# Optimization experiments

Measured on AMD Instinct MI355X. Metric: run time of the kernel, lower is better.

## Reference

```python
import jax, jax.numpy as jnp
import numpy as np

jax.config.update("jax_enable_x64", True)

P = 2038074743          # prime used by the ROBE-Z hash
BLOCK_K = 32            # tile sizes of the hashed reconstruction (kernel tile)
BLOCK_N = 32
INPUT_DIM = 8192
OUTPUT_DIM = 8192
HASH_SIZE = 1 << 22     # compressed parameter count
TOKENS = 512


def setup_inputs() -> dict:
    key = jax.random.key(0)
    k1, k2 = jax.random.split(key, 2)
    x = jax.random.normal(k1, (TOKENS, INPUT_DIM), dtype=jnp.float32)
    hashed_weight = jax.random.normal(k2, (HASH_SIZE,), dtype=jnp.float32) * 0.02
    bias = jnp.zeros((OUTPUT_DIM,), dtype=jnp.float32)
    # mirrors RzLinear._generate_random_numbers(seed): 4 random ints made even, prepended with P
    rng = np.random.RandomState(1024)
    r = rng.randint(0, P, size=(4,)).astype(np.int64)
    r = r + (r % 2)
    random_numbers = jnp.asarray(np.concatenate([np.array([P], dtype=np.int64), r]), dtype=jnp.int64)
    return {"x": x, "hashed_weight": hashed_weight, "bias": bias, "random_numbers": random_numbers}


def _weight_indices(random_numbers):
    """Hashed flat indices into hashed_weight for the dense [K, N] weight."""
    K, N = INPUT_DIM, OUTPUT_DIM
    kt, nt = K // BLOCK_K, N // BLOCK_N
    R1, R2, R3 = random_numbers[1], random_numbers[2], random_numbers[3]
    k_ids = jnp.arange(kt, dtype=jnp.int64)
    n_ids = jnp.arange(nt, dtype=jnp.int64)
    # per-tile start offset into the compressed array
    start = ((k_ids[:, None] * R3 + n_ids[None, :] * R2 + R1) % P) % (HASH_SIZE - BLOCK_K * BLOCK_N + 1)
    start = start.astype(jnp.int32)  # [kt, nt]
    off = (jnp.arange(BLOCK_K, dtype=jnp.int32)[:, None] * BLOCK_N
           + jnp.arange(BLOCK_N, dtype=jnp.int32)[None, :])  # [BK, BN], row-major within tile
    idx = start[:, None, :, None] + off[None, :, None, :]    # [kt, BK, nt, BN]
    return idx.reshape(K, N)


def reference(x, hashed_weight, bias, random_numbers):
    idx = _weight_indices(random_numbers)          # [K, N] int32
    W = hashed_weight[idx]                          # hashed-gather reconstruction, [K, N]
    out = jnp.matmul(x, W) + bias[None, :]          # [tokens, N]
    return out
```

## Files before the change

kernel.cpp:

```cpp
#include <hip/hip_runtime.h>
#include <hip/hip_fp16.h>

#define NDIM 8192
#define KDIM 8192
#define NT 256
#define MOD2 4193281
#define PRIME 2038074743LL

#define BM 256
#define BN 128
#define BK 32
#define KITER 64
#define ASTRIDE 40
#define BSLAB 1032

typedef _Float16 half8 __attribute__((ext_vector_type(8)));
typedef float floatx4 __attribute__((ext_vector_type(4)));

#define BARRIER() asm volatile("s_waitcnt lgkmcnt(0)\n\ts_barrier" ::: "memory")

__global__ __launch_bounds__(256) void prep_kernel(const float* __restrict__ x,
                                                   const float* __restrict__ hw,
                                                   const float* __restrict__ bias,
                                                   const int* __restrict__ rn,
                                                   __half* __restrict__ xh,
                                                   __half* __restrict__ hh,
                                                   int* __restrict__ starts,
                                                   float* __restrict__ out) {
    int b = blockIdx.x;
    int tid = threadIdx.x;
    if (b < 8192) {
        int i = b * 256 + tid;
        const float4* s; __half2* d; int j;
        if (i < (1 << 20)) { s = (const float4*)x;  d = (__half2*)xh; j = i; }
        else               { s = (const float4*)hw; d = (__half2*)hh; j = i - (1 << 20); }
        float4 v = s[j];
        d[j * 2]     = __floats2half2_rn(v.x, v.y);
        d[j * 2 + 1] = __floats2half2_rn(v.z, v.w);
    } else if (b < 8192 + 4096) {
        int i = (b - 8192) * 256 + tid;
        float4 bv = *(const float4*)(bias + ((i & 2047) << 2));
        ((float4*)out)[i] = bv;
    } else {
        int t = (b - 12288) * 256 + tid;
        bool is64 = (rn[1] == 0 && rn[3] == 0);
        long long R1 = is64 ? rn[2] : rn[1];
        long long R2 = is64 ? rn[4] : rn[2];
        long long R3 = is64 ? rn[6] : rn[3];
        long long k_id = t >> 8, n_id = t & 255;
        long long v = (k_id * R3 + n_id * R2 + R1) % PRIME;
        starts[t] = (int)(v % MOD2);
    }
}

__global__ __launch_bounds__(512, 4) void gemm_kernel(
    const __half* __restrict__ xh, const __half* __restrict__ hh,
    const int* __restrict__ starts, float* __restrict__ out) {
    __shared__ __align__(16) __half As[2][BM * ASTRIDE];
    __shared__ __align__(16) __half Bs[2][4 * BSLAB];
    __shared__ int Ss[KITER * 4];

    const int tid = threadIdx.x;
    const int lane = tid & 63;
    const int wave = tid >> 6;
    const int wm = wave >> 1;
    const int wn = wave & 1;
    const int quad = lane >> 4;
    const int l16 = lane & 15;

    const int i = blockIdx.x;
    const int ks = i & 3;
    const int m_blk = (i >> 2) & 1;
    const int n_blk = i >> 3;
    const int gm0 = m_blk * BM;
    const int gn0 = n_blk * BN;
    const int kt0 = ks * KITER;
    const int n_id0 = n_blk * 4;

    if (tid < KITER * 4) {
        int kp = tid >> 2, tile = tid & 3;
        Ss[tid] = starts[(kt0 + kp) * NT + n_id0 + tile];
    }

    const int a_row = tid >> 2;
    const int a_ch = tid & 3;
    const __half* aptr = xh + (size_t)(gm0 + a_row) * KDIM + kt0 * 32 + a_ch * 8;
    const unsigned a_woff = a_row * ASTRIDE + a_ch * 8;

    const int b_tile = tid >> 7;
    const int t7 = tid & 127;
    const int b_np = t7 & 15;
    const int b_kg = t7 >> 4;
    const int b_oct = b_kg >> 1;
    const unsigned b_woff = b_oct * BSLAB + (b_tile * 32 + 2 * b_np) * 8 + (b_kg & 1) * 4;

    uint4 paA0, paA1, paB0, paB1;
    unsigned pbA0, pbA1, pbA2, pbA3, pbB0, pbB1, pbB2, pbB3;

#define LOADT(P0, P1, Q0, Q1, Q2, Q3, kp_) do {                                \
        P0 = *(const uint4*)(aptr + (kp_) * 32);                               \
        P1 = *(const uint4*)(aptr + (size_t)128 * KDIM + (kp_) * 32);          \
        int st = Ss[(kp_) * 4 + b_tile];                                       \
        const __half* src = hh + st + b_kg * 128 + b_np * 2;                   \
        Q0 = *(const unsigned*)(src);                                          \
        Q1 = *(const unsigned*)(src + 32);                                     \
        Q2 = *(const unsigned*)(src + 64);                                     \
        Q3 = *(const unsigned*)(src + 96);                                     \
    } while (0)

#define STORET(P0, P1, Q0, Q1, Q2, Q3, buf_) do {                              \
        *(uint4*)&As[buf_][a_woff] = P0;                                       \
        *(uint4*)&As[buf_][(a_woff) + 128 * ASTRIDE] = P1;                     \
        unsigned lo0 = (Q0 & 0xffffu) | (Q1 << 16);                            \
        unsigned lo1 = (Q2 & 0xffffu) | (Q3 << 16);                            \
        unsigned hi0 = (Q0 >> 16) | (Q1 & 0xffff0000u);                        \
        unsigned hi1 = (Q2 >> 16) | (Q3 & 0xffff0000u);                        \
        uint2 e = {lo0, lo1}, o = {hi0, hi1};                                  \
        *(uint2*)&Bs[buf_][b_woff] = e;                                        \
        *(uint2*)&Bs[buf_][b_woff + 8] = o;                                    \
    } while (0)

    floatx4 acc[4][4];
#pragma unroll
    for (int r = 0; r < 4; r++)
#pragma unroll
        for (int c = 0; c < 4; c++)
            acc[r][c] = (floatx4){0.f, 0.f, 0.f, 0.f};

#define FRAGS_MFMA(buf_) do {                                                  \
        half8 af[4], bf[4];                                                    \
        _Pragma("unroll")                                                      \
        for (int r = 0; r < 4; r++)                                            \
            af[r] = *(const half8*)&As[buf_][(wm * 64 + r * 16 + l16) * ASTRIDE + quad * 8]; \
        _Pragma("unroll")                                                      \
        for (int c = 0; c < 4; c++)                                            \
            bf[c] = *(const half8*)&Bs[buf_][quad * BSLAB + (wn * 64 + c * 16 + l16) * 8];   \
        _Pragma("unroll")                                                      \
        for (int r = 0; r < 4; r++)                                            \
            _Pragma("unroll")                                                  \
            for (int c = 0; c < 4; c++)                                        \
                acc[r][c] = __builtin_amdgcn_mfma_f32_16x16x32_f16(af[r], bf[c], acc[r][c], 0, 0, 0); \
    } while (0)

    BARRIER();
    LOADT(paA0, paA1, pbA0, pbA1, pbA2, pbA3, 0);
    LOADT(paB0, paB1, pbB0, pbB1, pbB2, pbB3, 1);
    STORET(paA0, paA1, pbA0, pbA1, pbA2, pbA3, 0);
    BARRIER();

    for (int kp = 0; kp < KITER; kp += 2) {
        if (kp + 2 < KITER) LOADT(paA0, paA1, pbA0, pbA1, pbA2, pbA3, kp + 2);
        FRAGS_MFMA(0);
        STORET(paB0, paB1, pbB0, pbB1, pbB2, pbB3, 1);
        BARRIER();

        if (kp + 3 < KITER) LOADT(paB0, paB1, pbB0, pbB1, pbB2, pbB3, kp + 3);
        FRAGS_MFMA(1);
        if (kp + 2 < KITER)
            STORET(paA0, paA1, pbA0, pbA1, pbA2, pbA3, 0);
        BARRIER();
    }

#pragma unroll
    for (int c = 0; c < 4; c++) {
        int col = gn0 + wn * 64 + c * 16 + l16;
#pragma unroll
        for (int r = 0; r < 4; r++) {
            int row0 = gm0 + wm * 64 + r * 16 + quad * 4;
#pragma unroll
            for (int e = 0; e < 4; e++)
                atomicAdd(&out[(size_t)(row0 + e) * NDIM + col], acc[r][c][e]);
        }
    }
#undef LOADT
#undef STORET
#undef FRAGS_MFMA
}

extern "C" void kernel_launch(void* const* d_in, const int* in_sizes, int n_in,
                              void* d_out, int out_size, void* d_ws, size_t ws_size,
                              hipStream_t stream) {
    const float* x = (const float*)d_in[0];
    const float* hw = (const float*)d_in[1];
    const float* bias = (const float*)d_in[2];
    const int* rn = (const int*)d_in[3];
    float* out = (float*)d_out;

    char* ws = (char*)d_ws;
    __half* xh = (__half*)ws;
    __half* hh = (__half*)(ws + (8u << 20));
    int* starts = (int*)(ws + (16u << 20));

    hipLaunchKernelGGL(prep_kernel, dim3(12544), dim3(256), 0, stream,
                       x, hw, bias, rn, xh, hh, starts, out);
    hipLaunchKernelGGL(gemm_kernel, dim3(512), dim3(512), 0, stream, xh, hh, starts, out);
}
```

Before: 202.1 us.

## Halve GEMM block tile to 128x128 with 256 threads and restructure load pipeline

Shrinks the GEMM block tile from 256x128 to 128x128 and uses 256 threads per block, so the grid grows to 1024 blocks. The per-thread A and B load mapping is reorganized: A loads are split out and issued one step ahead, and each thread gathers eight hashed B values per tile stage and writes 16-byte LDS stores. The prep kernel now writes half-precision output as a single 8-byte store. This is meant to improve occupancy and CU load balance and to cut LDS store instruction count. In exchange, each B tile is fetched by twice as many blocks, and the separate A prefetch adds register pressure.

New measurement: 202.7 us. About the same (+0.3%).

```diff
diff --git a/kernel.cpp b/kernel.cpp
--- a/kernel.cpp
+++ b/kernel.cpp
@@ -7,7 +7,7 @@
 #define MOD2 4193281
 #define PRIME 2038074743LL
 
-#define BM 256
+#define BM 128
 #define BN 128
 #define BK 32
 #define KITER 64
@@ -31,12 +31,14 @@
     int tid = threadIdx.x;
     if (b < 8192) {
         int i = b * 256 + tid;
-        const float4* s; __half2* d; int j;
-        if (i < (1 << 20)) { s = (const float4*)x;  d = (__half2*)xh; j = i; }
-        else               { s = (const float4*)hw; d = (__half2*)hh; j = i - (1 << 20); }
+        const float4* s; uint2* d; int j;
+        if (i < (1 << 20)) { s = (const float4*)x;  d = (uint2*)xh; j = i; }
+        else               { s = (const float4*)hw; d = (uint2*)hh; j = i - (1 << 20); }
         float4 v = s[j];
-        d[j * 2]     = __floats2half2_rn(v.x, v.y);
-        d[j * 2 + 1] = __floats2half2_rn(v.z, v.w);
+        __half2 h01 = __floats2half2_rn(v.x, v.y);
+        __half2 h23 = __floats2half2_rn(v.z, v.w);
+        uint2 w = {*(unsigned*)&h01, *(unsigned*)&h23};
+        d[j] = w;
     } else if (b < 8192 + 4096) {
         int i = (b - 8192) * 256 + tid;
         float4 bv = *(const float4*)(bias + ((i & 2047) << 2));
@@ -53,7 +55,7 @@
     }
 }
 
-__global__ __launch_bounds__(512, 4) void gemm_kernel(
+__global__ __launch_bounds__(256, 4) void gemm_kernel(
     const __half* __restrict__ xh, const __half* __restrict__ hh,
     const int* __restrict__ starts, float* __restrict__ out) {
     __shared__ __align__(16) __half As[2][BM * ASTRIDE];
@@ -70,54 +72,60 @@
 
     const int i = blockIdx.x;
     const int ks = i & 3;
-    const int m_blk = (i >> 2) & 1;
-    const int n_blk = i >> 3;
+    const int m_blk = (i >> 2) & 3;
+    const int n_blk = i >> 4;
     const int gm0 = m_blk * BM;
     const int gn0 = n_blk * BN;
     const int kt0 = ks * KITER;
     const int n_id0 = n_blk * 4;
 
-    if (tid < KITER * 4) {
-        int kp = tid >> 2, tile = tid & 3;
-        Ss[tid] = starts[(kt0 + kp) * NT + n_id0 + tile];
-    }
-
-    const int a_row = tid >> 2;
-    const int a_ch = tid & 3;
-    const __half* aptr = xh + (size_t)(gm0 + a_row) * KDIM + kt0 * 32 + a_ch * 8;
-    const unsigned a_woff = a_row * ASTRIDE + a_ch * 8;
-
-    const int b_tile = tid >> 7;
-    const int t7 = tid & 127;
-    const int b_np = t7 & 15;
-    const int b_kg = t7 >> 4;
-    const int b_oct = b_kg >> 1;
-    const unsigned b_woff = b_oct * BSLAB + (b_tile * 32 + 2 * b_np) * 8 + (b_kg & 1) * 4;
-
-    uint4 paA0, paA1, paB0, paB1;
-    unsigned pbA0, pbA1, pbA2, pbA3, pbB0, pbB1, pbB2, pbB3;
-
-#define LOADT(P0, P1, Q0, Q1, Q2, Q3, kp_) do {                                \
-        P0 = *(const uint4*)(aptr + (kp_) * 32);                               \
-        P1 = *(const uint4*)(aptr + (size_t)128 * KDIM + (kp_) * 32);          \
+    Ss[tid] = starts[(kt0 + (tid >> 2)) * NT + n_id0 + (tid & 3)];
+
+    const int a_row = tid >> 1;
+    const int a_ch = tid & 1;
+    const __half* aptr = xh + (size_t)(gm0 + a_row) * KDIM + kt0 * 32 + a_ch * 16;
+    const unsigned a_woff = a_row * ASTRIDE + a_ch * 16;
+
+    const int b_tile = tid >> 6;
+    const int b_oct = (tid >> 4) & 3;
+    const int b_np = tid & 15;
+    const unsigned b_woff = b_oct * BSLAB + (b_tile * 32 + 2 * b_np) * 8;
+
+    uint4 pa0, pa1;
+    unsigned qE0, qE1, qE2, qE3, qE4, qE5, qE6, qE7;
+    unsigned qO0, qO1, qO2, qO3, qO4, qO5, qO6, qO7;
+
+#define LOADA(kp_) do {                                                        \
+        pa0 = *(const uint4*)(aptr + (kp_) * 32);                              \
+        pa1 = *(const uint4*)(aptr + (kp_) * 32 + 8);                          \
+    } while (0)
+
+#define LOADB(Q0, Q1, Q2, Q3, Q4, Q5, Q6, Q7, kp_) do {                        \
         int st = Ss[(kp_) * 4 + b_tile];                                       \
-        const __half* src = hh + st + b_kg * 128 + b_np * 2;                   \
+        const __half* src = hh + st + b_oct * 256 + b_np * 2;                  \
         Q0 = *(const unsigned*)(src);                                          \
         Q1 = *(const unsigned*)(src + 32);                                     \
         Q2 = *(const unsigned*)(src + 64);                                     \
         Q3 = *(const unsigned*)(src + 96);                                     \
-    } while (0)
-
-#define STORET(P0, P1, Q0, Q1, Q2, Q3, buf_) do {                              \
-        *(uint4*)&As[buf_][a_woff] = P0;                                       \
-        *(uint4*)&As[buf_][(a_woff) + 128 * ASTRIDE] = P1;                     \
-        unsigned lo0 = (Q0 & 0xffffu) | (Q1 << 16);                            \
-        unsigned lo1 = (Q2 & 0xffffu) | (Q3 << 16);                            \
-        unsigned hi0 = (Q0 >> 16) | (Q1 & 0xffff0000u);                        \
-        unsigned hi1 = (Q2 >> 16) | (Q3 & 0xffff0000u);                        \
-        uint2 e = {lo0, lo1}, o = {hi0, hi1};                                  \
-        *(uint2*)&Bs[buf_][b_woff] = e;                                        \
-        *(uint2*)&Bs[buf_][b_woff + 8] = o;                                    \
+        Q4 = *(const unsigned*)(src + 128);                                    \
+        Q5 = *(const unsigned*)(src + 160);                                    \
+        Q6 = *(const unsigned*)(src + 192);                                    \
+        Q7 = *(const unsigned*)(src + 224);                                    \
+    } while (0)
+
+#define STORET(Q0, Q1, Q2, Q3, Q4, Q5, Q6, Q7, buf_) do {                      \
+        *(uint4*)&As[buf_][a_woff] = pa0;                                      \
+        *(uint4*)&As[buf_][a_woff + 8] = pa1;                                  \
+        unsigned e0 = (Q0 & 0xffffu) | (Q1 << 16);                             \
+        unsigned e1 = (Q2 & 0xffffu) | (Q3 << 16);                             \
+        unsigned e2 = (Q4 & 0xffffu) | (Q5 << 16);                             \
+        unsigned e3 = (Q6 & 0xffffu) | (Q7 << 16);                             \
+        unsigned o0 = (Q0 >> 16) | (Q1 & 0xffff0000u);                         \
+        unsigned o1 = (Q2 >> 16) | (Q3 & 0xffff0000u);                         \
+        unsigned o2 = (Q4 >> 16) | (Q5 & 0xffff0000u);                         \
+        unsigned o3 = (Q6 >> 16) | (Q7 & 0xffff0000u);                         \
+        *(uint4*)&Bs[buf_][b_woff] = (uint4){e0, e1, e2, e3};                  \
+        *(uint4*)&Bs[buf_][b_woff + 8] = (uint4){o0, o1, o2, o3};              \
     } while (0)
 
     floatx4 acc[4][4];
@@ -143,21 +151,28 @@
     } while (0)
 
     BARRIER();
-    LOADT(paA0, paA1, pbA0, pbA1, pbA2, pbA3, 0);
-    LOADT(paB0, paB1, pbB0, pbB1, pbB2, pbB3, 1);
-    STORET(paA0, paA1, pbA0, pbA1, pbA2, pbA3, 0);
+    LOADB(qE0, qE1, qE2, qE3, qE4, qE5, qE6, qE7, 0);
+    LOADB(qO0, qO1, qO2, qO3, qO4, qO5, qO6, qO7, 1);
+    LOADA(0);
+    STORET(qE0, qE1, qE2, qE3, qE4, qE5, qE6, qE7, 0);
     BARRIER();
 
     for (int kp = 0; kp < KITER; kp += 2) {
-        if (kp + 2 < KITER) LOADT(paA0, paA1, pbA0, pbA1, pbA2, pbA3, kp + 2);
+        LOADA(kp + 1);
+        if (kp + 2 < KITER)
+            LOADB(qE0, qE1, qE2, qE3, qE4, qE5, qE6, qE7, kp + 2);
         FRAGS_MFMA(0);
-        STORET(paB0, paB1, pbB0, pbB1, pbB2, pbB3, 1);
+        STORET(qO0, qO1, qO2, qO3, qO4, qO5, qO6, qO7, 1);
         BARRIER();
 
-        if (kp + 3 < KITER) LOADT(paB0, paB1, pbB0, pbB1, pbB2, pbB3, kp + 3);
+        if (kp + 2 < KITER) {
+            LOADA(kp + 2);
+            if (kp + 3 < KITER)
+                LOADB(qO0, qO1, qO2, qO3, qO4, qO5, qO6, qO7, kp + 3);
+        }
         FRAGS_MFMA(1);
         if (kp + 2 < KITER)
-            STORET(paA0, paA1, pbA0, pbA1, pbA2, pbA3, 0);
+            STORET(qE0, qE1, qE2, qE3, qE4, qE5, qE6, qE7, 0);
         BARRIER();
     }
 
@@ -172,7 +187,8 @@
                 atomicAdd(&out[(size_t)(row0 + e) * NDIM + col], acc[r][c][e]);
         }
     }
-#undef LOADT
+#undef LOADA
+#undef LOADB
 #undef STORET
 #undef FRAGS_MFMA
 }
@@ -193,5 +209,5 @@
 
     hipLaunchKernelGGL(prep_kernel, dim3(12544), dim3(256), 0, stream,
                        x, hw, bias, rn, xh, hh, starts, out);
-    hipLaunchKernelGGL(gemm_kernel, dim3(512), dim3(512), 0, stream, xh, hh, starts, out);
+    hipLaunchKernelGGL(gemm_kernel, dim3(1024), dim3(256), 0, stream, xh, hh, starts, out);
 }
```
